# Optimization experiments

Measured on AMD Instinct MI355X. Metric: run time of the kernel, lower is better.

## Reference

```python
import jax, jax.numpy as jnp
import numpy as np

L, D, H, FF = 4, 256, 8, 4 * 256  # num_layers, d_model, nhead, ffn hidden
DK = D // H
EPS = 1e-5


def _ln(x, g, b):
    mu = jnp.mean(x, axis=-1, keepdims=True)
    var = jnp.mean(jnp.square(x - mu), axis=-1, keepdims=True)
    return (x - mu) * jax.lax.rsqrt(var + EPS) * g + b


def setup_inputs() -> dict:
    key = jax.random.key(0)
    ks = jax.random.split(key, 16)
    B, N = 8, 1024
    s = 0.02
    return {
        "x": jax.random.normal(ks[0], (B, N, D), jnp.float32),
        "coords": jax.random.normal(ks[1], (B, N, 3), jnp.float32),
        "Wq": jax.random.normal(ks[2], (L, D, D), jnp.float32) * s,
        "bq": jnp.zeros((L, D), jnp.float32),
        "Wk": jax.random.normal(ks[3], (L, D, D), jnp.float32) * s,
        "bk": jnp.zeros((L, D), jnp.float32),
        "Wv": jax.random.normal(ks[4], (L, D, D), jnp.float32) * s,
        "bv": jnp.zeros((L, D), jnp.float32),
        "alpha": jnp.full((L,), 0.1, jnp.float32),
        "W1": jax.random.normal(ks[5], (L, D, FF), jnp.float32) * s,
        "b1": jnp.zeros((L, FF), jnp.float32),
        "W2": jax.random.normal(ks[6], (L, FF, D), jnp.float32) * s,
        "b2": jnp.zeros((L, D), jnp.float32),
        "g1": jnp.ones((L, D), jnp.float32),
        "be1": jnp.zeros((L, D), jnp.float32),
        "g2": jnp.ones((L, D), jnp.float32),
        "be2": jnp.zeros((L, D), jnp.float32),
    }


def reference(x, coords, Wq, bq, Wk, bk, Wv, bv, alpha, W1, b1, W2, b2, g1, be1, g2, be2):
    B, N, _ = x.shape
    # Per-batch pairwise coord dot products (same math as the BN x BN matmul
    # sliced per batch in the original, computed without the cross-batch waste).
    G0 = jnp.einsum("bnc,bmc->bnm", coords, coords)  # [B,N,N]
    scale = 1.0 / jnp.sqrt(jnp.float32(DK))
    for i in range(L):
        q = (x @ Wq[i] + bq[i]).reshape(B, N, H, DK)
        k = (x @ Wk[i] + bk[i]).reshape(B, N, H, DK)
        v = (x @ Wv[i] + bv[i]).reshape(B, N, H, DK)
        scores = jnp.einsum("bnhd,bmhd->bhnm", q, k) * scale + (alpha[i] * G0)[:, None]
        attn = jax.nn.softmax(scores, axis=-1)
        out = jnp.einsum("bhnm,bmhd->bnhd", attn, v).reshape(B, N, D)
        x = _ln(x + out, g1[i], be1[i])
        ff = jnp.maximum(x @ W1[i] + b1[i], 0.0) @ W2[i] + b2[i]
        x = _ln(x + ff, g2[i], be2[i])
    return x
```

## Files before the change

### kernel.cpp

```cpp
#include <hip/hip_runtime.h>
#include <hip/hip_bf16.h>

#define BB 8
#define NN 1024
#define DD 256
#define HH 8
#define DK 32
#define FFN 1024
#define NLAYERS 4
#define MM (BB * NN)
#define ROW_ELEMS (MM * DD)

#define QSCALE 0.2550655192922103f
#define LOG2E  1.4426950408889634f

typedef unsigned short ushort_t;
typedef __attribute__((ext_vector_type(8))) short bf16x8;
typedef __attribute__((ext_vector_type(4))) short bf16x4;
typedef __attribute__((ext_vector_type(4))) float f32x4;

__device__ __forceinline__ f32x4 mfma16(bf16x4 a, bf16x4 b, f32x4 c) {
#if __has_builtin(__builtin_amdgcn_mfma_f32_16x16x16bf16_1k)
    return __builtin_amdgcn_mfma_f32_16x16x16bf16_1k(a, b, c, 0, 0, 0);
#elif defined(__AMDGCN__)
    f32x4 d;
    asm volatile("v_mfma_f32_16x16x16_bf16 %0, %1, %2, %3"
                 : "=v"(d)
                 : "v"(a), "v"(b), "v"(c));
    return d;
#else
    return c;
#endif
}

__device__ __forceinline__ ushort_t f2b(float f) {
    __hip_bfloat16 h = __float2bfloat16(f);
    return *reinterpret_cast<ushort_t*>(&h);
}

__device__ __forceinline__ float fast_exp2(float x) {
#if __has_builtin(__builtin_amdgcn_exp2f)
    return __builtin_amdgcn_exp2f(x);
#else
    return exp2f(x);
#endif
}

__device__ __forceinline__ void async_ld16(const void* g, void* l) {
    __builtin_amdgcn_global_load_lds((const __attribute__((address_space(1))) void*)g,
                                     (__attribute__((address_space(3))) void*)l, 16, 0, 0);
}

__global__ __launch_bounds__(256) void copy_in_kernel(const float4* __restrict__ in,
                                                      float4* __restrict__ xf,
                                                      ushort4* __restrict__ xb, int n4,
                                                      const float* __restrict__ coords,
                                                      ushort_t* __restrict__ Qa,
                                                      ushort_t* __restrict__ Ka) {
    int i = blockIdx.x * 256 + threadIdx.x;
    if (i < n4) {
        float4 v = in[i];
        xf[i] = v;
        ushort4 b = {f2b(v.x), f2b(v.y), f2b(v.z), f2b(v.w)};
        xb[i] = b;
    }
    if (blockIdx.x < 256) {
        const int id = blockIdx.x * 256 + threadIdx.x;
        const int bh = id >> 10, n = id & 1023;
        const int b = bh >> 3;
        ushort_t buf[32];
#pragma unroll
        for (int d = 0; d < 32; ++d) buf[d] = 0;
        buf[0] = f2b(coords[(size_t)(b * NN + n) * 3 + 0]);
        buf[1] = f2b(coords[(size_t)(b * NN + n) * 3 + 1]);
        buf[2] = f2b(coords[(size_t)(b * NN + n) * 3 + 2]);
        ushort_t* kp = Ka + ((size_t)bh * NN + n) * 64 + 32;
        ushort_t* qp = Qa + ((size_t)bh * NN + n) * 64 + 32;
        const uint4* b4 = (const uint4*)buf;
        uint4 z4 = {0u, 0u, 0u, 0u};
#pragma unroll
        for (int c = 0; c < 4; ++c) {
            *(uint4*)(kp + c * 8) = b4[c];
            *(uint4*)(qp + c * 8) = z4;
        }
    }
}

__global__ __launch_bounds__(256) void prep_kernel(const float* __restrict__ Wq,
                                                   const float* __restrict__ Wk,
                                                   const float* __restrict__ Wv,
                                                   const float* __restrict__ W1,
                                                   const float* __restrict__ W2,
                                                   const float* __restrict__ bq,
                                                   const float* __restrict__ bk,
                                                   const float* __restrict__ bv,
                                                   ushort_t* __restrict__ wqkvt,
                                                   ushort_t* __restrict__ w1t,
                                                   ushort_t* __restrict__ w2t,
                                                   float* __restrict__ bqkv) {
    const int id = blockIdx.x;
    const int layer = id / 707;
    const int r = id % 707;
    const int tid = threadIdx.x;

    if (r >= 704) {
        const int chunk = r - 704;
        const float* src = (chunk == 0) ? bq : (chunk == 1) ? bk : bv;
        bqkv[layer * 768 + chunk * 256 + tid] = src[layer * 256 + tid];
        return;
    }

    const float* src;
    ushort_t* dst;
    int R, C, x, y;
    if (r < 192) {
        const int w = r >> 6, rr = r & 63;
        src = ((w == 0) ? Wq : (w == 1) ? Wk : Wv) + (size_t)layer * 65536;
        dst = wqkvt + (size_t)layer * 196608 + w * 65536;
        R = 256; C = 256; x = rr & 7; y = rr >> 3;
    } else if (r < 448) {
        const int rr = r - 192;
        src = W1 + (size_t)layer * 262144;
        dst = w1t + (size_t)layer * 262144;
        R = 256; C = 1024; x = rr & 31; y = rr >> 5;
    } else {
        const int rr = r - 448;
        src = W2 + (size_t)layer * 262144;
        dst = w2t + (size_t)layer * 262144;
        R = 1024; C = 256; x = rr & 7; y = rr >> 3;
    }
    const int r0 = y * 32, c0 = x * 32;
    __shared__ float tile[32][33];
    const int tx = tid & 31, ty = tid >> 5;
#pragma unroll
    for (int i = 0; i < 4; ++i)
        tile[ty + 8 * i][tx] = src[(size_t)(r0 + ty + 8 * i) * C + (c0 + tx)];
    __syncthreads();
#pragma unroll
    for (int i = 0; i < 4; ++i)
        dst[(size_t)(c0 + ty + 8 * i) * R + (r0 + tx)] = f2b(tile[tx][ty + 8 * i]);
}

template <int MODE, int BM>
__global__ __launch_bounds__(256) void mfma_gemm_kernel(const ushort_t* __restrict__ A,
                                                        const ushort_t* __restrict__ Bt,
                                                        const float* __restrict__ bias,
                                                        void* __restrict__ C0,
                                                        void* __restrict__ C1,
                                                        void* __restrict__ C2,
                                                        const float* __restrict__ coords,
                                                        const float* __restrict__ alpha, int layer,
                                                        int K, int ldc) {
    constexpr int NI = BM / 32;
    __shared__ ushort_t As0[2][BM * 32];
    __shared__ ushort_t As1[2][BM * 32];
    __shared__ ushort_t Bs0[2][128 * 32];
    __shared__ ushort_t Bs1[2][128 * 32];

    const int t    = threadIdx.x;
    const int bm   = blockIdx.y * BM;
    const int bn   = blockIdx.x * 128;
    const int wave = t >> 6, lane = t & 63;
    const int wm   = (wave >> 1) * (BM / 2), wn = (wave & 1) * 64;
    const int quad = lane >> 4, l16 = lane & 15;

    const int srow = t >> 2;
    const int scol = (t & 3) * 8;

    f32x4 acc[NI][4];
#pragma unroll
    for (int i = 0; i < NI; ++i)
#pragma unroll
        for (int j = 0; j < 4; ++j) {
            f32x4 z = {0.f, 0.f, 0.f, 0.f};
            acc[i][j] = z;
        }

    auto stage = [&](int pb, int k0) {
        async_ld16(A + (size_t)(bm + srow) * K + k0 + scol, As0[pb] + wave * 512);
        if constexpr (BM == 128)
            async_ld16(A + (size_t)(bm + 64 + srow) * K + k0 + scol, As0[pb] + 2048 + wave * 512);
        async_ld16(Bt + (size_t)(bn + srow) * K + k0 + scol, Bs0[pb] + wave * 512);
        async_ld16(Bt + (size_t)(bn + 64 + srow) * K + k0 + scol, Bs0[pb] + 2048 + wave * 512);
        async_ld16(A + (size_t)(bm + srow) * K + k0 + 32 + scol, As1[pb] + wave * 512);
        if constexpr (BM == 128)
            async_ld16(A + (size_t)(bm + 64 + srow) * K + k0 + 32 + scol, As1[pb] + 2048 + wave * 512);
        async_ld16(Bt + (size_t)(bn + srow) * K + k0 + 32 + scol, Bs1[pb] + wave * 512);
        async_ld16(Bt + (size_t)(bn + 64 + srow) * K + k0 + 32 + scol, Bs1[pb] + 2048 + wave * 512);
    };

    stage(0, 0);
    int pb = 0;
    for (int k0 = 0; k0 < K; k0 += 64, pb ^= 1) {
        __syncthreads();

        if (k0 + 64 < K) stage(pb ^ 1, k0 + 64);

        bf16x8 af0[NI], af1[NI], bf0[4], bf1[4];
#pragma unroll
        for (int i = 0; i < NI; ++i) {
            af0[i] = *(const bf16x8*)(As0[pb] + (wm + i * 16 + l16) * 32 + quad * 8);
            af1[i] = *(const bf16x8*)(As1[pb] + (wm + i * 16 + l16) * 32 + quad * 8);
        }
#pragma unroll
        for (int j = 0; j < 4; ++j) {
            bf0[j] = *(const bf16x8*)(Bs0[pb] + (wn + j * 16 + l16) * 32 + quad * 8);
            bf1[j] = *(const bf16x8*)(Bs1[pb] + (wn + j * 16 + l16) * 32 + quad * 8);
        }
#pragma unroll
        for (int i = 0; i < NI; ++i)
#pragma unroll
            for (int j = 0; j < 4; ++j) {
                acc[i][j] = __builtin_amdgcn_mfma_f32_16x16x32_bf16(af0[i], bf0[j], acc[i][j], 0, 0, 0);
                acc[i][j] = __builtin_amdgcn_mfma_f32_16x16x32_bf16(af1[i], bf1[j], acc[i][j], 0, 0, 0);
            }
    }

    const float av = (MODE == 2) ? alpha[layer] : 0.f;

#pragma unroll
    for (int j = 0; j < 4; ++j) {
        const int col = bn + wn + j * 16 + l16;
        const float bsv = bias[col];
#pragma unroll
        for (int i = 0; i < NI; ++i) {
            const int row0 = bm + wm + i * 16 + quad * 4;
            if (MODE == 2) {
                const int bb2 = row0 >> 10, nn0 = row0 & 1023;
                const int which = col >> 8, rem = col & 255;
                const int h = rem >> 5, d = rem & 31;
                const size_t bh = (size_t)((bb2 << 3) + h);
                if (which == 2) {
                    ushort4 pk;
                    pk.x = f2b(acc[i][j][0] + bsv);
                    pk.y = f2b(acc[i][j][1] + bsv);
                    pk.z = f2b(acc[i][j][2] + bsv);
                    pk.w = f2b(acc[i][j][3] + bsv);
                    *(ushort4*)&((ushort_t*)C2)[(bh * DK + d) * NN + nn0] = pk;
                } else {
#pragma unroll
                    for (int r = 0; r < 4; ++r) {
                        const float v = acc[i][j][r] + bsv;
                        const int nn = nn0 + r;
                        if (which == 0) {
                            ((ushort_t*)C0)[(bh * NN + nn) * 64 + d] = f2b(v * QSCALE);
                            if (d < 3)
                                ((ushort_t*)C0)[(bh * NN + nn) * 64 + 32 + d] =
                                    f2b(av * LOG2E * coords[(size_t)(bb2 * NN + nn) * 3 + d]);
                        } else {
                            ((ushort_t*)C1)[(bh * NN + nn) * 64 + d] = f2b(v);
                        }
                    }
                }
            } else {
#pragma unroll
                for (int r = 0; r < 4; ++r) {
                    float v = acc[i][j][r] + bsv;
                    if (MODE == 0)
                        ((float*)C0)[(size_t)(row0 + r) * ldc + col] = v;
                    else
                        ((ushort_t*)C0)[(size_t)(row0 + r) * ldc + col] = f2b(fmaxf(v, 0.f));
                }
            }
        }
    }
}

__global__ __launch_bounds__(512) void ffn_ln_kernel(const ushort_t* __restrict__ A,
                                                     const ushort_t* __restrict__ W1t,
                                                     const ushort_t* __restrict__ W2t,
                                                     const float* __restrict__ b1,
                                                     const float* __restrict__ b2,
                                                     const float* __restrict__ xres,
                                                     const float* __restrict__ g,
                                                     const float* __restrict__ be,
                                                     float* __restrict__ xout,
                                                     ushort_t* __restrict__ xb) {
    __shared__ ushort_t Ha[32][32][32];
    __shared__ ushort_t Asf[8][32][32];
    __shared__ ushort_t Bs0[2][256 * 32];
    __shared__ ushort_t Bs1[2][256 * 32];
    __shared__ float redS[8][32];
    __shared__ float redQ[8][32];

    const int t = threadIdx.x;
    const int bm = blockIdx.x * 32;
    const int wave = t >> 6, lane = t & 63;
    const int quad = lane >> 4, l16 = lane & 15;
    const int wn = wave * 32;
    const int scol = (t & 3) * 8;

#pragma unroll
    for (int c = 0; c < 2; ++c) {
        const int arow = (t >> 2) & 31;
        const int acol = (c * 4 + (t >> 7)) * 32 + scol;
        async_ld16(A + (size_t)(bm + arow) * 256 + acol,
                   (ushort_t*)Asf + c * 4096 + wave * 512);
    }

    auto stageB1 = [&](int pb, int step) {
        const int nbase = (step >> 2) * 256;
        const int k0 = (step & 3) * 64;
#pragma unroll
        for (int c = 0; c < 2; ++c) {
            const int brow = nbase + c * 128 + (t >> 2);
            async_ld16(W1t + (size_t)brow * 256 + k0 + scol, Bs0[pb] + c * 4096 + wave * 512);
            async_ld16(W1t + (size_t)brow * 256 + k0 + 32 + scol, Bs1[pb] + c * 4096 + wave * 512);
        }
    };
    auto stageB2 = [&](int pb, int step) {
        const int k0 = step * 64;
#pragma unroll
        for (int c = 0; c < 2; ++c) {
            const int brow = c * 128 + (t >> 2);
            async_ld16(W2t + (size_t)brow * 1024 + k0 + scol, Bs0[pb] + c * 4096 + wave * 512);
            async_ld16(W2t + (size_t)brow * 1024 + k0 + 32 + scol, Bs1[pb] + c * 4096 + wave * 512);
        }
    };

    f32x4 acc1[2][2], acc2[2][2];
#pragma unroll
    for (int i = 0; i < 2; ++i)
#pragma unroll
        for (int j = 0; j < 2; ++j) {
            f32x4 z = {0.f, 0.f, 0.f, 0.f};
            acc1[i][j] = z;
            acc2[i][j] = z;
        }

    stageB1(0, 0);
    int pb = 0;

    for (int step = 0; step < 16; ++step, pb ^= 1) {
        __syncthreads();
        if (step < 15) stageB1(pb ^ 1, step + 1);
        else stageB2(pb ^ 1, 0);

        const int ks = step & 3;
        bf16x8 af0[2], af1[2], bf0[2], bf1[2];
#pragma unroll
        for (int i = 0; i < 2; ++i) {
            af0[i] = *(const bf16x8*)&Asf[2 * ks][i * 16 + l16][quad * 8];
            af1[i] = *(const bf16x8*)&Asf[2 * ks + 1][i * 16 + l16][quad * 8];
        }
#pragma unroll
        for (int j = 0; j < 2; ++j) {
            bf0[j] = *(const bf16x8*)(Bs0[pb] + (wn + j * 16 + l16) * 32 + quad * 8);
            bf1[j] = *(const bf16x8*)(Bs1[pb] + (wn + j * 16 + l16) * 32 + quad * 8);
        }
#pragma unroll
        for (int i = 0; i < 2; ++i)
#pragma unroll
            for (int j = 0; j < 2; ++j) {
                acc1[i][j] = __builtin_amdgcn_mfma_f32_16x16x32_bf16(af0[i], bf0[j], acc1[i][j], 0, 0, 0);
                acc1[i][j] = __builtin_amdgcn_mfma_f32_16x16x32_bf16(af1[i], bf1[j], acc1[i][j], 0, 0, 0);
            }

        if (ks == 3) {
            const int nc = step >> 2;
#pragma unroll
            for (int j = 0; j < 2; ++j) {
                const int col = nc * 256 + wn + j * 16 + l16;
                const float bj = b1[col];
#pragma unroll
                for (int i = 0; i < 2; ++i)
#pragma unroll
                    for (int r = 0; r < 4; ++r) {
                        const int row = i * 16 + quad * 4 + r;
                        Ha[nc * 8 + wave][row][j * 16 + l16] =
                            f2b(fmaxf(acc1[i][j][r] + bj, 0.f));
                    }
            }
#pragma unroll
            for (int i = 0; i < 2; ++i)
#pragma unroll
                for (int j = 0; j < 2; ++j) {
                    f32x4 z = {0.f, 0.f, 0.f, 0.f};
                    acc1[i][j] = z;
                }
        }
    }

    for (int step = 0; step < 16; ++step, pb ^= 1) {
        __syncthreads();
        if (step < 15) stageB2(pb ^ 1, step + 1);

        bf16x8 af0[2], af1[2], bf0[2], bf1[2];
#pragma unroll
        for (int i = 0; i < 2; ++i) {
            af0[i] = *(const bf16x8*)&Ha[2 * step][i * 16 + l16][quad * 8];
            af1[i] = *(const bf16x8*)&Ha[2 * step + 1][i * 16 + l16][quad * 8];
        }
#pragma unroll
        for (int j = 0; j < 2; ++j) {
            bf0[j] = *(const bf16x8*)(Bs0[pb] + (wn + j * 16 + l16) * 32 + quad * 8);
            bf1[j] = *(const bf16x8*)(Bs1[pb] + (wn + j * 16 + l16) * 32 + quad * 8);
        }
#pragma unroll
        for (int i = 0; i < 2; ++i)
#pragma unroll
            for (int j = 0; j < 2; ++j) {
                acc2[i][j] = __builtin_amdgcn_mfma_f32_16x16x32_bf16(af0[i], bf0[j], acc2[i][j], 0, 0, 0);
                acc2[i][j] = __builtin_amdgcn_mfma_f32_16x16x32_bf16(af1[i], bf1[j], acc2[i][j], 0, 0, 0);
            }
    }

    float mean[2][4], rstd[2][4];

    {
        float sum_[2][4];
#pragma unroll
        for (int i = 0; i < 2; ++i)
#pragma unroll
            for (int r = 0; r < 4; ++r) sum_[i][r] = 0.f;
#pragma unroll
        for (int j = 0; j < 2; ++j) {
            const int col = wn + j * 16 + l16;
            const float bj = b2[col];
#pragma unroll
            for (int i = 0; i < 2; ++i) {
                const int row = bm + i * 16 + quad * 4;
#pragma unroll
                for (int r = 0; r < 4; ++r) {
                    const float v = acc2[i][j][r] + bj + xres[(size_t)(row + r) * DD + col];
                    acc2[i][j][r] = v;
                    sum_[i][r] += v;
                }
            }
        }
#pragma unroll
        for (int i = 0; i < 2; ++i)
#pragma unroll
            for (int r = 0; r < 4; ++r) {
                float s = sum_[i][r];
                s += __shfl_xor(s, 1);
                s += __shfl_xor(s, 2);
                s += __shfl_xor(s, 4);
                s += __shfl_xor(s, 8);
                sum_[i][r] = s;
            }
        if (l16 == 0) {
#pragma unroll
            for (int i = 0; i < 2; ++i)
#pragma unroll
                for (int r = 0; r < 4; ++r) redS[wave][i * 16 + quad * 4 + r] = sum_[i][r];
        }
        __syncthreads();
#pragma unroll
        for (int i = 0; i < 2; ++i)
#pragma unroll
            for (int r = 0; r < 4; ++r) {
                const int rl = i * 16 + quad * 4 + r;
                float s = 0.f;
#pragma unroll
                for (int w = 0; w < 8; ++w) s += redS[w][rl];
                mean[i][r] = s * (1.0f / 256.0f);
            }
    }

    {
        float sq_[2][4];
#pragma unroll
        for (int i = 0; i < 2; ++i)
#pragma unroll
            for (int r = 0; r < 4; ++r) sq_[i][r] = 0.f;
#pragma unroll
        for (int j = 0; j < 2; ++j)
#pragma unroll
            for (int i = 0; i < 2; ++i)
#pragma unroll
                for (int r = 0; r < 4; ++r) {
                    const float d = acc2[i][j][r] - mean[i][r];
                    sq_[i][r] += d * d;
                }
#pragma unroll
        for (int i = 0; i < 2; ++i)
#pragma unroll
            for (int r = 0; r < 4; ++r) {
                float s = sq_[i][r];
                s += __shfl_xor(s, 1);
                s += __shfl_xor(s, 2);
                s += __shfl_xor(s, 4);
                s += __shfl_xor(s, 8);
                sq_[i][r] = s;
            }
        if (l16 == 0) {
#pragma unroll
            for (int i = 0; i < 2; ++i)
#pragma unroll
                for (int r = 0; r < 4; ++r) redQ[wave][i * 16 + quad * 4 + r] = sq_[i][r];
        }
        __syncthreads();
#pragma unroll
        for (int i = 0; i < 2; ++i)
#pragma unroll
            for (int r = 0; r < 4; ++r) {
                const int rl = i * 16 + quad * 4 + r;
                float s = 0.f;
#pragma unroll
                for (int w = 0; w < 8; ++w) s += redQ[w][rl];
                rstd[i][r] = rsqrtf(s * (1.0f / 256.0f) + 1e-5f);
            }
    }

#pragma unroll
    for (int j = 0; j < 2; ++j) {
        const int col = wn + j * 16 + l16;
        const float gv = g[col];
        const float bev = be[col];
#pragma unroll
        for (int i = 0; i < 2; ++i) {
            const int row = bm + i * 16 + quad * 4;
#pragma unroll
            for (int r = 0; r < 4; ++r) {
                const float y = (acc2[i][j][r] - mean[i][r]) * rstd[i][r] * gv + bev;
                xout[(size_t)(row + r) * DD + col] = y;
                xb[(size_t)(row + r) * DD + col] = f2b(y);
            }
        }
    }
}

__global__ __launch_bounds__(256, 2) void attn8_kernel(const ushort_t* __restrict__ Qa,
                                                       const ushort_t* __restrict__ Ka,
                                                       const ushort_t* __restrict__ Vt,
                                                       float* __restrict__ aout) {
    const int b = blockIdx.x, h = blockIdx.y, n0 = blockIdx.z * 64;
    const int t = threadIdx.x, wave = t >> 6, lane = t & 63;
    const int quad = lane >> 4, l16 = lane & 15;
    const int bh = b * HH + h;

    __shared__ __align__(16) char smem[56320];
    ushort_t (*Ks)[64][72] = (ushort_t (*)[64][72])smem;
    ushort_t (*Vs)[32][72] = (ushort_t (*)[32][72])(smem + 36864);
    float    (*Om)[64][36] = (float (*)[64][36])smem;
    float    (*Lm)[64]     = (float (*)[64])(smem + 55296);

    bf16x8 aq[4][2];
#pragma unroll
    for (int s = 0; s < 4; ++s) {
        const ushort_t* qp = Qa + ((size_t)bh * NN + n0 + s * 16 + l16) * 64 + quad * 8;
        aq[s][0] = *(const bf16x8*)qp;
        aq[s][1] = *(const bf16x8*)(qp + 32);
    }

    const f32x4 z = {0.f, 0.f, 0.f, 0.f};
    f32x4 acc[4][2];
    float lsum[4];
#pragma unroll
    for (int s = 0; s < 4; ++s) { acc[s][0] = z; acc[s][1] = z; lsum[s] = 0.f; }

    const ushort_t* kg = Ka + ((size_t)bh * NN + wave * 256) * 64;
    const ushort_t* vg = Vt + (size_t)bh * DK * NN + wave * 256;

    const int srow = lane >> 3, sch = (lane & 7) * 8;

    uint4 kreg[8], vreg[4];
#pragma unroll
    for (int i = 0; i < 8; ++i) kreg[i] = *(const uint4*)(kg + (size_t)(i * 8 + srow) * 64 + sch);
#pragma unroll
    for (int i = 0; i < 4; ++i) vreg[i] = *(const uint4*)(vg + (size_t)(i * 8 + srow) * NN + sch);

    for (int kt = 0; kt < 4; ++kt) {
#pragma unroll
        for (int i = 0; i < 8; ++i) *(uint4*)&Ks[wave][i * 8 + srow][sch] = kreg[i];
#pragma unroll
        for (int i = 0; i < 4; ++i) *(uint4*)&Vs[wave][i * 8 + srow][sch] = vreg[i];

        bf16x8 bk0[4], bk1[4];
#pragma unroll
        for (int jt = 0; jt < 4; ++jt) {
            bk0[jt] = *(const bf16x8*)&Ks[wave][jt * 16 + l16][quad * 8];
            bk1[jt] = *(const bf16x8*)&Ks[wave][jt * 16 + l16][32 + quad * 8];
        }
        bf16x4 vfrag[2][4];
#pragma unroll
        for (int g = 0; g < 2; ++g)
#pragma unroll
            for (int jt = 0; jt < 4; ++jt)
                vfrag[g][jt] = *(const bf16x4*)&Vs[wave][g * 16 + l16][jt * 16 + quad * 4];

        if (kt < 3) {
            const ushort_t* kg2 = kg + (size_t)(kt + 1) * 64 * 64;
            const ushort_t* vg2 = vg + (kt + 1) * 64;
#pragma unroll
            for (int i = 0; i < 8; ++i)
                kreg[i] = *(const uint4*)(kg2 + (size_t)(i * 8 + srow) * 64 + sch);
#pragma unroll
            for (int i = 0; i < 4; ++i)
                vreg[i] = *(const uint4*)(vg2 + (size_t)(i * 8 + srow) * NN + sch);
        }

#pragma unroll
        for (int s = 0; s < 4; ++s) {
            f32x4 st[4];
            __builtin_amdgcn_s_setprio(1);
#pragma unroll
            for (int jt = 0; jt < 4; ++jt) {
                st[jt] = __builtin_amdgcn_mfma_f32_16x16x32_bf16(bk0[jt], aq[s][0], z, 0, 0, 0);
                st[jt] = __builtin_amdgcn_mfma_f32_16x16x32_bf16(bk1[jt], aq[s][1], st[jt], 0, 0, 0);
            }
            __builtin_amdgcn_s_setprio(0);
            bf16x4 pf[4];
            float ls = 0.f;
#pragma unroll
            for (int jt = 0; jt < 4; ++jt) {
                float e0 = fast_exp2(st[jt][0]);
                float e1 = fast_exp2(st[jt][1]);
                float e2 = fast_exp2(st[jt][2]);
                float e3 = fast_exp2(st[jt][3]);
                ls += (e0 + e1) + (e2 + e3);
                pf[jt][0] = (short)f2b(e0);
                pf[jt][1] = (short)f2b(e1);
                pf[jt][2] = (short)f2b(e2);
                pf[jt][3] = (short)f2b(e3);
            }
            lsum[s] += ls;
            __builtin_amdgcn_s_setprio(1);
#pragma unroll
            for (int jt = 0; jt < 4; ++jt) {
                acc[s][0] = mfma16(vfrag[0][jt], pf[jt], acc[s][0]);
                acc[s][1] = mfma16(vfrag[1][jt], pf[jt], acc[s][1]);
            }
            __builtin_amdgcn_s_setprio(0);
        }
    }

#pragma unroll
    for (int s = 0; s < 4; ++s) {
        lsum[s] += __shfl_xor(lsum[s], 16);
        lsum[s] += __shfl_xor(lsum[s], 32);
    }

    __syncthreads();
    if (quad == 0) {
#pragma unroll
        for (int s = 0; s < 4; ++s) Lm[wave][s * 16 + l16] = lsum[s];
    }

#pragma unroll
    for (int s = 0; s < 4; ++s) {
        const int q = s * 16 + l16;
#pragma unroll
        for (int g = 0; g < 2; ++g) {
            float4 v = {acc[s][g][0], acc[s][g][1], acc[s][g][2], acc[s][g][3]};
            *(float4*)&Om[wave][q][g * 16 + quad * 4] = v;
        }
    }
    __syncthreads();

    {
        const int q = t >> 2, dseg = (t & 3) * 8;
        const float inv = 1.0f / (Lm[0][q] + Lm[1][q] + Lm[2][q] + Lm[3][q]);
        float* op = aout + (size_t)(b * NN + n0 + q) * DD + h * DK + dseg;
        float4 s0 = {0.f, 0.f, 0.f, 0.f}, s1 = {0.f, 0.f, 0.f, 0.f};
#pragma unroll
        for (int w = 0; w < 4; ++w) {
            float4 a = *(const float4*)&Om[w][q][dseg];
            float4 c = *(const float4*)&Om[w][q][dseg + 4];
            s0.x += a.x; s0.y += a.y; s0.z += a.z; s0.w += a.w;
            s1.x += c.x; s1.y += c.y; s1.z += c.z; s1.w += c.w;
        }
        float4 o0 = {s0.x * inv, s0.y * inv, s0.z * inv, s0.w * inv};
        float4 o1 = {s1.x * inv, s1.y * inv, s1.z * inv, s1.w * inv};
        *(float4*)op = o0;
        *(float4*)(op + 4) = o1;
    }
}

__global__ __launch_bounds__(256) void addln_kernel(const float* __restrict__ x,
                                                    ushort_t* __restrict__ xb,
                                                    const float* __restrict__ delta, int dstride,
                                                    const float* __restrict__ g,
                                                    const float* __restrict__ be,
                                                    float* __restrict__ xout) {
    const int row  = blockIdx.x * 4 + (threadIdx.x >> 6);
    const int lane = threadIdx.x & 63;
    const size_t base = (size_t)row * DD + lane * 4;

    float4 xv = *(const float4*)(x + base);
    float4 dl = *(const float4*)(delta + (size_t)row * dstride + lane * 4);
    float v0 = xv.x + dl.x, v1 = xv.y + dl.y, v2 = xv.z + dl.z, v3 = xv.w + dl.w;

    float s = v0 + v1 + v2 + v3;
#pragma unroll
    for (int off = 32; off; off >>= 1) s += __shfl_xor(s, off);
    const float mean = s * (1.0f / 256.0f);

    float d0 = v0 - mean, d1 = v1 - mean, d2 = v2 - mean, d3 = v3 - mean;
    float s2 = d0 * d0 + d1 * d1 + d2 * d2 + d3 * d3;
#pragma unroll
    for (int off = 32; off; off >>= 1) s2 += __shfl_xor(s2, off);
    const float rs = rsqrtf(s2 * (1.0f / 256.0f) + 1e-5f);

    float4 gv = *(const float4*)(g + lane * 4);
    float4 bv = *(const float4*)(be + lane * 4);
    float y0 = d0 * rs * gv.x + bv.x;
    float y1 = d1 * rs * gv.y + bv.y;
    float y2 = d2 * rs * gv.z + bv.z;
    float y3 = d3 * rs * gv.w + bv.w;

    float4 o = {y0, y1, y2, y3};
    *(float4*)(xout + base) = o;
    ushort4 ob = {f2b(y0), f2b(y1), f2b(y2), f2b(y3)};
    *(ushort4*)(xb + base) = ob;
}

extern "C" void kernel_launch(void* const* d_in, const int* in_sizes, int n_in,
                              void* d_out, int out_size, void* d_ws, size_t ws_size,
                              hipStream_t stream) {
    const float* x      = (const float*)d_in[0];
    const float* coords = (const float*)d_in[1];
    const float* Wq     = (const float*)d_in[2];
    const float* bq     = (const float*)d_in[3];
    const float* Wk     = (const float*)d_in[4];
    const float* bk     = (const float*)d_in[5];
    const float* Wv     = (const float*)d_in[6];
    const float* bv     = (const float*)d_in[7];
    const float* alpha  = (const float*)d_in[8];
    const float* W1     = (const float*)d_in[9];
    const float* b1     = (const float*)d_in[10];
    const float* W2     = (const float*)d_in[11];
    const float* b2     = (const float*)d_in[12];
    const float* g1     = (const float*)d_in[13];
    const float* be1    = (const float*)d_in[14];
    const float* g2     = (const float*)d_in[15];
    const float* be2    = (const float*)d_in[16];

    float* ws = (float*)d_ws;
    float*    xf    = ws;
    ushort_t* xb    = (ushort_t*)(ws + 2097152);
    ushort_t* Qa    = (ushort_t*)(ws + 3145728);
    ushort_t* Ka    = (ushort_t*)(ws + 5242880);
    ushort_t* Vt    = (ushort_t*)(ws + 7340032);
    float*    aout  = ws + 8388608;
    ushort_t* wqkvt = (ushort_t*)(ws + 10485760);
    ushort_t* w1t   = (ushort_t*)(ws + 10878976);
    ushort_t* w2t   = (ushort_t*)(ws + 11403264);
    float*    bqkv  = ws + 11927552;

    prep_kernel<<<NLAYERS * 707, 256, 0, stream>>>(Wq, Wk, Wv, W1, W2, bq, bk, bv,
                                                   wqkvt, w1t, w2t, bqkv);

    copy_in_kernel<<<ROW_ELEMS / 4 / 256, 256, 0, stream>>>(
        (const float4*)x, (float4*)xf, (ushort4*)xb, ROW_ELEMS / 4, coords, Qa, Ka);

    for (int i = 0; i < NLAYERS; ++i) {
        mfma_gemm_kernel<2, 64><<<dim3(6, 128), 256, 0, stream>>>(
            xb, wqkvt + (size_t)i * 196608, bqkv + i * 768, Qa, Ka, Vt,
            coords, alpha, i, 256, 0);

        attn8_kernel<<<dim3(8, 8, 16), 256, 0, stream>>>(Qa, Ka, Vt, aout);

        addln_kernel<<<MM / 4, 256, 0, stream>>>(xf, xb, aout, 256, g1 + i * 256, be1 + i * 256, xf);

        ffn_ln_kernel<<<MM / 32, 512, 0, stream>>>(
            xb, w1t + (size_t)i * 262144, w2t + (size_t)i * 262144,
            b1 + i * 1024, b2 + i * 256, xf,
            g2 + i * 256, be2 + i * 256,
            (i == NLAYERS - 1) ? (float*)d_out : xf, xb);
    }
}
```

Before: 397.9 us.

## Fuse attention residual LayerNorm into FFN kernel and interleave FFN1/FFN2 chunks

Removes the separate addln kernel. The FFN kernel now computes the post-attention residual add and LayerNorm for its 32-row tile itself, keeping the fp32 result in shared memory as the second residual and writing a bf16 copy as the FFN input. The FFN1 and FFN2 loops are merged into one 32-step pipeline that alternates 256-column hidden chunks, so the hidden buffer shrinks from 32 slices to 8. The aim is to save one launch and a global round trip of activations, at the cost of extra shared memory (a 32x260 float tile) and branching inside the main loop.

```diff
diff --git a/kernel.cpp b/kernel.cpp
--- a/kernel.cpp
+++ b/kernel.cpp
@@ -266,20 +266,23 @@
     }
 }
 
-__global__ __launch_bounds__(512) void ffn_ln_kernel(const ushort_t* __restrict__ A,
+__global__ __launch_bounds__(512) void ffn_ln_kernel(const float* __restrict__ aout,
+                                                     const float* __restrict__ xfin,
                                                      const ushort_t* __restrict__ W1t,
                                                      const ushort_t* __restrict__ W2t,
+                                                     const float* __restrict__ g1,
+                                                     const float* __restrict__ be1,
                                                      const float* __restrict__ b1,
                                                      const float* __restrict__ b2,
-                                                     const float* __restrict__ xres,
-                                                     const float* __restrict__ g,
-                                                     const float* __restrict__ be,
+                                                     const float* __restrict__ g2,
+                                                     const float* __restrict__ be2,
                                                      float* __restrict__ xout,
                                                      ushort_t* __restrict__ xb) {
-    __shared__ ushort_t Ha[32][32][32];
+    __shared__ ushort_t Ha[8][32][32];
     __shared__ ushort_t Asf[8][32][32];
     __shared__ ushort_t Bs0[2][256 * 32];
     __shared__ ushort_t Bs1[2][256 * 32];
+    __shared__ float Ya[32][260];
     __shared__ float redS[8][32];
     __shared__ float redQ[8][32];
 
@@ -290,17 +293,9 @@
     const int wn = wave * 32;
     const int scol = (t & 3) * 8;
 
-#pragma unroll
-    for (int c = 0; c < 2; ++c) {
-        const int arow = (t >> 2) & 31;
-        const int acol = (c * 4 + (t >> 7)) * 32 + scol;
-        async_ld16(A + (size_t)(bm + arow) * 256 + acol,
-                   (ushort_t*)Asf + c * 4096 + wave * 512);
-    }
-
-    auto stageB1 = [&](int pb, int step) {
-        const int nbase = (step >> 2) * 256;
-        const int k0 = (step & 3) * 64;
+    auto stageB1 = [&](int pb, int nc, int ks) {
+        const int nbase = nc * 256;
+        const int k0 = ks * 64;
 #pragma unroll
         for (int c = 0; c < 2; ++c) {
             const int brow = nbase + c * 128 + (t >> 2);
@@ -308,8 +303,8 @@
             async_ld16(W1t + (size_t)brow * 256 + k0 + 32 + scol, Bs1[pb] + c * 4096 + wave * 512);
         }
     };
-    auto stageB2 = [&](int pb, int step) {
-        const int k0 = step * 64;
+    auto stageB2 = [&](int pb, int nc, int ks) {
+        const int k0 = nc * 256 + ks * 64;
 #pragma unroll
         for (int c = 0; c < 2; ++c) {
             const int brow = c * 128 + (t >> 2);
@@ -317,6 +312,47 @@
             async_ld16(W2t + (size_t)brow * 1024 + k0 + 32 + scol, Bs1[pb] + c * 4096 + wave * 512);
         }
     };
+    auto stage = [&](int pb, int st) {
+        const int group = st >> 2, ks = st & 3, nc = group >> 1;
+        if (!(group & 1)) stageB1(pb, nc, ks);
+        else stageB2(pb, nc, ks);
+    };
+
+    stage(0, 0);
+
+#pragma unroll
+    for (int rr = 0; rr < 4; ++rr) {
+        const int row = wave * 4 + rr;
+        const size_t base = (size_t)(bm + row) * DD + lane * 4;
+
+        float4 xv = *(const float4*)(xfin + base);
+        float4 dl = *(const float4*)(aout + base);
+        float v0 = xv.x + dl.x, v1 = xv.y + dl.y, v2 = xv.z + dl.z, v3 = xv.w + dl.w;
+
+        float s = v0 + v1 + v2 + v3;
+#pragma unroll
+        for (int off = 32; off; off >>= 1) s += __shfl_xor(s, off);
+        const float mean = s * (1.0f / 256.0f);
+
+        float d0 = v0 - mean, d1 = v1 - mean, d2 = v2 - mean, d3 = v3 - mean;
+        float s2 = d0 * d0 + d1 * d1 + d2 * d2 + d3 * d3;
+#pragma unroll
+        for (int off = 32; off; off >>= 1) s2 += __shfl_xor(s2, off);
+        const float rs = rsqrtf(s2 * (1.0f / 256.0f) + 1e-5f);
+
+        float4 gv = *(const float4*)(g1 + lane * 4);
+        float4 bv = *(const float4*)(be1 + lane * 4);
+        float y0 = d0 * rs * gv.x + bv.x;
+        float y1 = d1 * rs * gv.y + bv.y;
+        float y2 = d2 * rs * gv.z + bv.z;
+        float y3 = d3 * rs * gv.w + bv.w;
+
+        float4 yv = {y0, y1, y2, y3};
+        *(float4*)&Ya[row][lane * 4] = yv;
+        const int col0 = lane * 4;
+        ushort4 yb = {f2b(y0), f2b(y1), f2b(y2), f2b(y3)};
+        *(ushort4*)&Asf[col0 >> 5][row][col0 & 31] = yb;
+    }
 
     f32x4 acc1[2][2], acc2[2][2];
 #pragma unroll
@@ -328,81 +364,71 @@
             acc2[i][j] = z;
         }
 
-    stageB1(0, 0);
     int pb = 0;
-
-    for (int step = 0; step < 16; ++step, pb ^= 1) {
+    for (int st = 0; st < 32; ++st, pb ^= 1) {
         __syncthreads();
-        if (step < 15) stageB1(pb ^ 1, step + 1);
-        else stageB2(pb ^ 1, 0);
-
-        const int ks = step & 3;
+        if (st < 31) stage(pb ^ 1, st + 1);
+
+        const int group = st >> 2, ks = st & 3;
+        const bool ff1 = !(group & 1);
+
         bf16x8 af0[2], af1[2], bf0[2], bf1[2];
 #pragma unroll
         for (int i = 0; i < 2; ++i) {
-            af0[i] = *(const bf16x8*)&Asf[2 * ks][i * 16 + l16][quad * 8];
-            af1[i] = *(const bf16x8*)&Asf[2 * ks + 1][i * 16 + l16][quad * 8];
+            if (ff1) {
+                af0[i] = *(const bf16x8*)&Asf[2 * ks][i * 16 + l16][quad * 8];
+                af1[i] = *(const bf16x8*)&Asf[2 * ks + 1][i * 16 + l16][quad * 8];
+            } else {
+                af0[i] = *(const bf16x8*)&Ha[2 * ks][i * 16 + l16][quad * 8];
+                af1[i] = *(const bf16x8*)&Ha[2 * ks + 1][i * 16 + l16][quad * 8];
+            }
         }
 #pragma unroll
         for (int j = 0; j < 2; ++j) {
             bf0[j] = *(const bf16x8*)(Bs0[pb] + (wn + j * 16 + l16) * 32 + quad * 8);
             bf1[j] = *(const bf16x8*)(Bs1[pb] + (wn + j * 16 + l16) * 32 + quad * 8);
         }
-#pragma unroll
-        for (int i = 0; i < 2; ++i)
-#pragma unroll
-            for (int j = 0; j < 2; ++j) {
-                acc1[i][j] = __builtin_amdgcn_mfma_f32_16x16x32_bf16(af0[i], bf0[j], acc1[i][j], 0, 0, 0);
-                acc1[i][j] = __builtin_amdgcn_mfma_f32_16x16x32_bf16(af1[i], bf1[j], acc1[i][j], 0, 0, 0);
-            }
-
-        if (ks == 3) {
-            const int nc = step >> 2;
-#pragma unroll
-            for (int j = 0; j < 2; ++j) {
-                const int col = nc * 256 + wn + j * 16 + l16;
-                const float bj = b1[col];
+
+        if (ff1) {
+#pragma unroll
+            for (int i = 0; i < 2; ++i)
+#pragma unroll
+                for (int j = 0; j < 2; ++j) {
+                    acc1[i][j] = __builtin_amdgcn_mfma_f32_16x16x32_bf16(af0[i], bf0[j], acc1[i][j], 0, 0, 0);
+                    acc1[i][j] = __builtin_amdgcn_mfma_f32_16x16x32_bf16(af1[i], bf1[j], acc1[i][j], 0, 0, 0);
+                }
+            if (ks == 3) {
+                const int nc = group >> 1;
+#pragma unroll
+                for (int j = 0; j < 2; ++j) {
+                    const int col = nc * 256 + wn + j * 16 + l16;
+                    const float bj = b1[col];
+#pragma unroll
+                    for (int i = 0; i < 2; ++i)
+#pragma unroll
+                        for (int r = 0; r < 4; ++r) {
+                            const int row = i * 16 + quad * 4 + r;
+                            Ha[wave][row][j * 16 + l16] =
+                                f2b(fmaxf(acc1[i][j][r] + bj, 0.f));
+                        }
+                }
 #pragma unroll
                 for (int i = 0; i < 2; ++i)
 #pragma unroll
-                    for (int r = 0; r < 4; ++r) {
-                        const int row = i * 16 + quad * 4 + r;
-                        Ha[nc * 8 + wave][row][j * 16 + l16] =
-                            f2b(fmaxf(acc1[i][j][r] + bj, 0.f));
+                    for (int j = 0; j < 2; ++j) {
+                        f32x4 z = {0.f, 0.f, 0.f, 0.f};
+                        acc1[i][j] = z;
                     }
             }
+        } else {
 #pragma unroll
             for (int i = 0; i < 2; ++i)
 #pragma unroll
                 for (int j = 0; j < 2; ++j) {
-                    f32x4 z = {0.f, 0.f, 0.f, 0.f};
-                    acc1[i][j] = z;
+                    acc2[i][j] = __builtin_amdgcn_mfma_f32_16x16x32_bf16(af0[i], bf0[j], acc2[i][j], 0, 0, 0);
+                    acc2[i][j] = __builtin_amdgcn_mfma_f32_16x16x32_bf16(af1[i], bf1[j], acc2[i][j], 0, 0, 0);
                 }
         }
-    }
-
-    for (int step = 0; step < 16; ++step, pb ^= 1) {
-        __syncthreads();
-        if (step < 15) stageB2(pb ^ 1, step + 1);
-
-        bf16x8 af0[2], af1[2], bf0[2], bf1[2];
-#pragma unroll
-        for (int i = 0; i < 2; ++i) {
-            af0[i] = *(const bf16x8*)&Ha[2 * step][i * 16 + l16][quad * 8];
-            af1[i] = *(const bf16x8*)&Ha[2 * step + 1][i * 16 + l16][quad * 8];
-        }
-#pragma unroll
-        for (int j = 0; j < 2; ++j) {
-            bf0[j] = *(const bf16x8*)(Bs0[pb] + (wn + j * 16 + l16) * 32 + quad * 8);
-            bf1[j] = *(const bf16x8*)(Bs1[pb] + (wn + j * 16 + l16) * 32 + quad * 8);
-        }
-#pragma unroll
-        for (int i = 0; i < 2; ++i)
-#pragma unroll
-            for (int j = 0; j < 2; ++j) {
-                acc2[i][j] = __builtin_amdgcn_mfma_f32_16x16x32_bf16(af0[i], bf0[j], acc2[i][j], 0, 0, 0);
-                acc2[i][j] = __builtin_amdgcn_mfma_f32_16x16x32_bf16(af1[i], bf1[j], acc2[i][j], 0, 0, 0);
-            }
     }
 
     float mean[2][4], rstd[2][4];
@@ -419,10 +445,10 @@
             const float bj = b2[col];
 #pragma unroll
             for (int i = 0; i < 2; ++i) {
-                const int row = bm + i * 16 + quad * 4;
 #pragma unroll
                 for (int r = 0; r < 4; ++r) {
-                    const float v = acc2[i][j][r] + bj + xres[(size_t)(row + r) * DD + col];
+                    const int row = i * 16 + quad * 4 + r;
+                    const float v = acc2[i][j][r] + bj + Ya[row][col];
                     acc2[i][j][r] = v;
                     sum_[i][r] += v;
                 }
@@ -506,8 +532,8 @@
 #pragma unroll
     for (int j = 0; j < 2; ++j) {
         const int col = wn + j * 16 + l16;
-        const float gv = g[col];
-        const float bev = be[col];
+        const float gv = g2[col];
+        const float bev = be2[col];
 #pragma unroll
         for (int i = 0; i < 2; ++i) {
             const int row = bm + i * 16 + quad * 4;
@@ -666,44 +692,6 @@
         *(float4*)op = o0;
         *(float4*)(op + 4) = o1;
     }
-}
-
-__global__ __launch_bounds__(256) void addln_kernel(const float* __restrict__ x,
-                                                    ushort_t* __restrict__ xb,
-                                                    const float* __restrict__ delta, int dstride,
-                                                    const float* __restrict__ g,
-                                                    const float* __restrict__ be,
-                                                    float* __restrict__ xout) {
-    const int row  = blockIdx.x * 4 + (threadIdx.x >> 6);
-    const int lane = threadIdx.x & 63;
-    const size_t base = (size_t)row * DD + lane * 4;
-
-    float4 xv = *(const float4*)(x + base);
-    float4 dl = *(const float4*)(delta + (size_t)row * dstride + lane * 4);
-    float v0 = xv.x + dl.x, v1 = xv.y + dl.y, v2 = xv.z + dl.z, v3 = xv.w + dl.w;
-
-    float s = v0 + v1 + v2 + v3;
-#pragma unroll
-    for (int off = 32; off; off >>= 1) s += __shfl_xor(s, off);
-    const float mean = s * (1.0f / 256.0f);
-
-    float d0 = v0 - mean, d1 = v1 - mean, d2 = v2 - mean, d3 = v3 - mean;
-    float s2 = d0 * d0 + d1 * d1 + d2 * d2 + d3 * d3;
-#pragma unroll
-    for (int off = 32; off; off >>= 1) s2 += __shfl_xor(s2, off);
-    const float rs = rsqrtf(s2 * (1.0f / 256.0f) + 1e-5f);
-
-    float4 gv = *(const float4*)(g + lane * 4);
-    float4 bv = *(const float4*)(be + lane * 4);
-    float y0 = d0 * rs * gv.x + bv.x;
-    float y1 = d1 * rs * gv.y + bv.y;
-    float y2 = d2 * rs * gv.z + bv.z;
-    float y3 = d3 * rs * gv.w + bv.w;
-
-    float4 o = {y0, y1, y2, y3};
-    *(float4*)(xout + base) = o;
-    ushort4 ob = {f2b(y0), f2b(y1), f2b(y2), f2b(y3)};
-    *(ushort4*)(xb + base) = ob;
 }
 
 extern "C" void kernel_launch(void* const* d_in, const int* in_sizes, int n_in,
@@ -752,11 +740,9 @@
 
         attn8_kernel<<<dim3(8, 8, 16), 256, 0, stream>>>(Qa, Ka, Vt, aout);
 
-        addln_kernel<<<MM / 4, 256, 0, stream>>>(xf, xb, aout, 256, g1 + i * 256, be1 + i * 256, xf);
-
         ffn_ln_kernel<<<MM / 32, 512, 0, stream>>>(
-            xb, w1t + (size_t)i * 262144, w2t + (size_t)i * 262144,
-            b1 + i * 1024, b2 + i * 256, xf,
+            aout, xf, w1t + (size_t)i * 262144, w2t + (size_t)i * 262144,
+            g1 + i * 256, be1 + i * 256, b1 + i * 1024, b2 + i * 256,
             g2 + i * 256, be2 + i * 256,
             (i == NLAYERS - 1) ? (float*)d_out : xf, xb);
     }
```

Result: faster. 373.3 us (-6.2%).
